# Kernel optimization log

Hardware: AMD Instinct MI355X
Metric: run time of the kernel (lower is better)

The kernel has to match this reference:

```python
import jax, jax.numpy as jnp
import numpy as np

SEQ, D_IN, D_OUT = 8192, 768, 64


def setup_inputs() -> dict:
    key = jax.random.key(0)
    k0, k1, k2, k3 = jax.random.split(key, 4)
    x = jax.random.normal(k0, (SEQ, D_IN), dtype=jnp.float32)
    # nn.Linear default init ~ U(-1/sqrt(d_in), 1/sqrt(d_in)); small scale keeps softmax stable
    s = 0.02
    Wq = jax.random.normal(k1, (D_IN, D_OUT), dtype=jnp.float32) * s
    Wk = jax.random.normal(k2, (D_IN, D_OUT), dtype=jnp.float32) * s
    Wv = jax.random.normal(k3, (D_IN, D_OUT), dtype=jnp.float32) * s
    return {"x": x, "Wq": Wq, "Wk": Wk, "Wv": Wv}


def reference(x, Wq, Wk, Wv):
    # queries/keys/values: [S, d_out]
    q = x @ Wq
    k = x @ Wk
    v = x @ Wv
    d_k = k.shape[-1]
    scores = q @ k.T / jnp.sqrt(jnp.asarray(d_k, x.dtype))  # [S, S]
    weights = jax.nn.softmax(scores, axis=-1)
    return weights @ v  # [S, d_out]
```

## Files before the change

### kernel.cpp

```cpp
#include <hip/hip_runtime.h>
#include <hip/hip_bf16.h>

#define SEQ  8192
#define DIN  768
#define DOUT 64

typedef __attribute__((ext_vector_type(8))) short short8;
typedef __attribute__((ext_vector_type(4))) short s16x4;
typedef __attribute__((ext_vector_type(4))) float f32x4;

__device__ inline unsigned short f2bf(float f) {
    __hip_bfloat16 h = __float2bfloat16(f);
    return __builtin_bit_cast(unsigned short, h);
}

__global__ __launch_bounds__(256) void wconv_kernel(
    const float* __restrict__ Wq, const float* __restrict__ Wk,
    const float* __restrict__ Wv, unsigned short* __restrict__ Wt) {
    int idx = blockIdx.x * 256 + threadIdx.x;
    int c = idx / DIN;
    int k = idx - c * DIN;
    int sel = c >> 6, cc = c & 63;
    const float* W = (sel == 0) ? Wq : ((sel == 1) ? Wk : Wv);
    float v = W[k * DOUT + cc];
    if (sel == 0) v *= 0.125f * 1.4426950408889634f;
    Wt[c * DIN + k] = f2bf(v);
}

__global__ __launch_bounds__(256) void proj_kernel(
    const float* __restrict__ x, const unsigned short* __restrict__ Wt,
    unsigned short* __restrict__ Q8, unsigned short* __restrict__ Kf,
    unsigned short* __restrict__ Vf) {
    __shared__ unsigned short xs[16 * 72];
    __shared__ unsigned short ws[192 * 72];

    const int tid  = threadIdx.x;
    const int m0   = blockIdx.x * 16;
    const int lane = tid & 63;
    const int w    = tid >> 6;
    const int g    = lane >> 4;
    const int l15  = lane & 15;

    f32x4 zero = {0.f, 0.f, 0.f, 0.f};
    f32x4 acc[3] = {zero, zero, zero};

    for (int kt = 0; kt < 12; ++kt) {
        const int k0 = kt * 64;
        {
            int r = tid >> 4, c4 = (tid & 15) * 4;
            float4 f = *reinterpret_cast<const float4*>(&x[(m0 + r) * DIN + k0 + c4]);
            s16x4 o4;
            o4[0] = (short)f2bf(f.x); o4[1] = (short)f2bf(f.y);
            o4[2] = (short)f2bf(f.z); o4[3] = (short)f2bf(f.w);
            *(s16x4*)&xs[r * 72 + c4] = o4;
        }
#pragma unroll
        for (int p = 0; p < 6; ++p) {
            int c    = p * 32 + (tid >> 3);
            int col8 = (tid & 7) * 8;
            *(short8*)&ws[c * 72 + col8] =
                *(const short8*)&Wt[c * DIN + k0 + col8];
        }
        __syncthreads();
        short8 a0 = *(short8*)&xs[l15 * 72 + g * 8];
        short8 a1 = *(short8*)&xs[l15 * 72 + g * 8 + 32];
#pragma unroll
        for (int i = 0; i < 3; ++i) {
            int nt = w * 3 + i;
            short8 b0 = *(short8*)&ws[(nt * 16 + l15) * 72 + g * 8];
            short8 b1 = *(short8*)&ws[(nt * 16 + l15) * 72 + g * 8 + 32];
            acc[i] = __builtin_amdgcn_mfma_f32_16x16x32_bf16(a0, b0, acc[i], 0, 0, 0);
            acc[i] = __builtin_amdgcn_mfma_f32_16x16x32_bf16(a1, b1, acc[i], 0, 0, 0);
        }
        __syncthreads();
    }
#pragma unroll
    for (int i = 0; i < 3; ++i) {
#pragma unroll
        for (int r = 0; r < 4; ++r) {
            int row = m0 + g * 4 + r;
            int col = (w * 3 + i) * 16 + l15;
            unsigned short b = f2bf(acc[i][r]);
            if (col < 64) {
                Q8[row * 64 + col] = b;
            } else if (col < 128) {
                int d  = col - 64;
                int t  = row >> 6, nt = (row >> 4) & 3, lk = row & 15;
                int h  = d >> 5, kg = (d >> 3) & 3, e = d & 7;
                Kf[(((t * 4 + nt) * 2 + h) * 64 + kg * 16 + lk) * 8 + e] = b;
            } else {
                int d  = col - 128;
                int kv = row;
                int t  = kv >> 6, k6 = kv & 63;
                int c  = k6 >> 5, r5 = k6 & 31;
                int hf = r5 >> 4, vg = (r5 >> 2) & 3, j = (r5 & 3) + hf * 4;
                int dn = d >> 4, lv = d & 15;
                Vf[(((t * 2 + c) * 4 + dn) * 64 + vg * 16 + lv) * 8 + j] = b;
            }
        }
    }
}

__global__ __launch_bounds__(256, 4) void flash_kernel(
    const unsigned short* __restrict__ Q8, const unsigned short* __restrict__ Kf,
    const unsigned short* __restrict__ Vf, float* __restrict__ Op,
    float* __restrict__ Mp, float* __restrict__ Lp, int ntiles) {
    const int tid  = threadIdx.x;
    const int w    = tid >> 6;
    const int lane = tid & 63;
    const int g    = lane >> 4;
    const int l15  = lane & 15;
    const int q0   = (blockIdx.x * 4 + w) * 32;
    const int nsub = ntiles * 2;
    const int sub0 = blockIdx.y * nsub;

    short8 qa[4];
#pragma unroll
    for (int qg = 0; qg < 2; ++qg) {
        qa[qg * 2 + 0] = *(const short8*)&Q8[(q0 + qg * 16 + l15) * 64 + g * 8];
        qa[qg * 2 + 1] = *(const short8*)&Q8[(q0 + qg * 16 + l15) * 64 + g * 8 + 32];
    }

    f32x4 zero = {0.f, 0.f, 0.f, 0.f};
    f32x4 o[2][4];
    float m[2]  = {-3e38f, -3e38f};
    float ln[2] = {0.f, 0.f};
#pragma unroll
    for (int qg = 0; qg < 2; ++qg)
#pragma unroll
        for (int dn = 0; dn < 4; ++dn) o[qg][dn] = zero;

    const unsigned short* kfp = Kf + (size_t)sub0 * 2048 + lane * 8;
    const unsigned short* vfp = Vf + (size_t)sub0 * 2048 + lane * 8;

    short8 kb[2][2];
#pragma unroll
    for (int nt = 0; nt < 2; ++nt)
#pragma unroll
        for (int h = 0; h < 2; ++h)
            kb[nt][h] = *(const short8*)&kfp[(nt * 2 + h) * 512];

    for (int i = 0; i < nsub; ++i) {
        f32x4 s[2][2];
#pragma unroll
        for (int qg = 0; qg < 2; ++qg)
#pragma unroll
            for (int nt = 0; nt < 2; ++nt) s[qg][nt] = zero;
#pragma unroll
        for (int nt = 0; nt < 2; ++nt) {
            s[0][nt] = __builtin_amdgcn_mfma_f32_16x16x32_bf16(kb[nt][0], qa[0], s[0][nt], 0, 0, 0);
            s[0][nt] = __builtin_amdgcn_mfma_f32_16x16x32_bf16(kb[nt][1], qa[1], s[0][nt], 0, 0, 0);
            s[1][nt] = __builtin_amdgcn_mfma_f32_16x16x32_bf16(kb[nt][0], qa[2], s[1][nt], 0, 0, 0);
            s[1][nt] = __builtin_amdgcn_mfma_f32_16x16x32_bf16(kb[nt][1], qa[3], s[1][nt], 0, 0, 0);
        }

        short8 vf[4];
#pragma unroll
        for (int dn = 0; dn < 4; ++dn)
            vf[dn] = *(const short8*)&vfp[(size_t)i * 2048 + dn * 512];

#pragma unroll
        for (int nt = 0; nt < 2; ++nt)
#pragma unroll
            for (int h = 0; h < 2; ++h)
                kb[nt][h] = *(const short8*)&kfp[(size_t)(i + 1) * 2048 + (nt * 2 + h) * 512];

        short8 pa[2];
#pragma unroll
        for (int qg = 0; qg < 2; ++qg) {
            float pm = fmaxf(
                fmaxf(fmaxf(s[qg][0][0], s[qg][0][1]), fmaxf(s[qg][0][2], s[qg][0][3])),
                fmaxf(fmaxf(s[qg][1][0], s[qg][1][1]), fmaxf(s[qg][1][2], s[qg][1][3])));
            if (__any(pm > m[qg] + 8.f)) {
                pm = fmaxf(pm, __shfl_xor(pm, 16));
                pm = fmaxf(pm, __shfl_xor(pm, 32));
                float mn = fmaxf(m[qg], pm);
                float a  = __builtin_amdgcn_exp2f(m[qg] - mn);
                m[qg] = mn;
                ln[qg] *= a;
#pragma unroll
                for (int dn = 0; dn < 4; ++dn) o[qg][dn] *= a;
            }
            float p[8];
#pragma unroll
            for (int nt = 0; nt < 2; ++nt)
#pragma unroll
                for (int r = 0; r < 4; ++r)
                    p[nt * 4 + r] = __builtin_amdgcn_exp2f(s[qg][nt][r] - m[qg]);
            ln[qg] += ((p[0] + p[1]) + (p[2] + p[3])) + ((p[4] + p[5]) + (p[6] + p[7]));
            short8 pk;
#pragma unroll
            for (int j = 0; j < 8; ++j) pk[j] = (short)f2bf(p[j]);
            pa[qg] = pk;
        }

#pragma unroll
        for (int dn = 0; dn < 4; ++dn) {
            o[0][dn] = __builtin_amdgcn_mfma_f32_16x16x32_bf16(vf[dn], pa[0], o[0][dn], 0, 0, 0);
            o[1][dn] = __builtin_amdgcn_mfma_f32_16x16x32_bf16(vf[dn], pa[1], o[1][dn], 0, 0, 0);
        }
    }

    const size_t sb = (size_t)blockIdx.y * SEQ;
#pragma unroll
    for (int qg = 0; qg < 2; ++qg) {
        float ps = ln[qg];
        ps += __shfl_xor(ps, 16);
        ps += __shfl_xor(ps, 32);
#pragma unroll
        for (int dn = 0; dn < 4; ++dn)
            *(f32x4*)&Op[(sb + q0 + qg * 16 + l15) * 64 + dn * 16 + 4 * g] = o[qg][dn];
        if (g == 0) {
            Mp[sb + q0 + qg * 16 + l15] = m[qg];
            Lp[sb + q0 + qg * 16 + l15] = ps;
        }
    }
}

__global__ __launch_bounds__(256) void reduce_kernel(
    const float* __restrict__ Op, const float* __restrict__ Mp,
    const float* __restrict__ Lp, float* __restrict__ Out, int NS) {
    int q = blockIdx.x * 4 + (threadIdx.x >> 6);
    int d = threadIdx.x & 63;
    float M = -3e38f;
    for (int s = 0; s < NS; ++s) M = fmaxf(M, Mp[s * SEQ + q]);
    float L = 0.f, acc = 0.f;
    for (int s = 0; s < NS; ++s) {
        float w = __builtin_amdgcn_exp2f(Mp[s * SEQ + q] - M);
        L   += Lp[s * SEQ + q] * w;
        acc += Op[((size_t)s * SEQ + q) * 64 + d] * w;
    }
    Out[q * 64 + d] = acc / L;
}

extern "C" void kernel_launch(void* const* d_in, const int* in_sizes, int n_in,
                              void* d_out, int out_size, void* d_ws, size_t ws_size,
                              hipStream_t stream) {
    const float* x  = (const float*)d_in[0];
    const float* Wq = (const float*)d_in[1];
    const float* Wk = (const float*)d_in[2];
    const float* Wv = (const float*)d_in[3];
    float* out = (float*)d_out;

    char* ws = (char*)d_ws;
    unsigned short* Wt = (unsigned short*)(ws);
    unsigned short* Q8 = (unsigned short*)(ws + 294912);
    unsigned short* Kf = (unsigned short*)(ws + 294912 + 1048576);
    unsigned short* Vf = (unsigned short*)(ws + 294912 + 2097152);
    const size_t fixed = 294912 + 3 * 1048576;

    int NS = 16;
    while (NS > 1 && fixed + (size_t)NS * (2097152 + 65536) > ws_size) NS >>= 1;
    float* Op = (float*)(ws + fixed);
    float* Mp = (float*)(ws + fixed + (size_t)NS * 2097152);
    float* Lp = (float*)(ws + fixed + (size_t)NS * 2097152 + (size_t)NS * 32768);
    const int ntiles = SEQ / (NS * 64);

    wconv_kernel<<<dim3(576), dim3(256), 0, stream>>>(Wq, Wk, Wv, Wt);
    proj_kernel<<<dim3(512), dim3(256), 0, stream>>>(x, Wt, Q8, Kf, Vf);
    flash_kernel<<<dim3(64, NS), dim3(256), 0, stream>>>(Q8, Kf, Vf, Op, Mp, Lp, ntiles);
    reduce_kernel<<<dim3(2048), dim3(256), 0, stream>>>(Op, Mp, Lp, out, NS);
}
```

Before: 61.54 us.

## Share K/V tiles via double-buffered LDS in flash kernel; enlarge projection row tile

In the flash kernel, each wave used to load the full K and V subtiles from global memory on its own. Now the four waves load one quarter each into double-buffered shared memory and synchronise every iteration, which cuts global/L2 traffic by four at the cost of a block barrier per subtile. The projection kernel now handles 32 rows per block instead of 16, with each wave covering 6 output column tiles. This halves the number of redundant weight-tile loads and the grid size. The per-iteration __syncthreads may reduce latency hiding, and the flash kernel now uses extra LDS, which could limit occupancy.

Measured after the change: 81.32 us. +32.1%, slower.

```diff
diff --git a/kernel.cpp b/kernel.cpp
--- a/kernel.cpp
+++ b/kernel.cpp
@@ -31,28 +31,31 @@
     const float* __restrict__ x, const unsigned short* __restrict__ Wt,
     unsigned short* __restrict__ Q8, unsigned short* __restrict__ Kf,
     unsigned short* __restrict__ Vf) {
-    __shared__ unsigned short xs[16 * 72];
+    __shared__ unsigned short xs[32 * 72];
     __shared__ unsigned short ws[192 * 72];
 
     const int tid  = threadIdx.x;
-    const int m0   = blockIdx.x * 16;
+    const int m0   = blockIdx.x * 32;
     const int lane = tid & 63;
     const int w    = tid >> 6;
+    const int rh   = w & 1;
+    const int ch   = w >> 1;
     const int g    = lane >> 4;
     const int l15  = lane & 15;
 
     f32x4 zero = {0.f, 0.f, 0.f, 0.f};
-    f32x4 acc[3] = {zero, zero, zero};
+    f32x4 acc[6] = {zero, zero, zero, zero, zero, zero};
 
     for (int kt = 0; kt < 12; ++kt) {
         const int k0 = kt * 64;
         {
-            int r = tid >> 4, c4 = (tid & 15) * 4;
-            float4 f = *reinterpret_cast<const float4*>(&x[(m0 + r) * DIN + k0 + c4]);
-            s16x4 o4;
-            o4[0] = (short)f2bf(f.x); o4[1] = (short)f2bf(f.y);
-            o4[2] = (short)f2bf(f.z); o4[3] = (short)f2bf(f.w);
-            *(s16x4*)&xs[r * 72 + c4] = o4;
+            int r = tid >> 3, c8 = (tid & 7) * 8;
+            const float4* src4 = reinterpret_cast<const float4*>(&x[(m0 + r) * DIN + k0 + c8]);
+            float4 f0 = src4[0], f1 = src4[1];
+            short8 o8;
+            o8[0]=(short)f2bf(f0.x); o8[1]=(short)f2bf(f0.y); o8[2]=(short)f2bf(f0.z); o8[3]=(short)f2bf(f0.w);
+            o8[4]=(short)f2bf(f1.x); o8[5]=(short)f2bf(f1.y); o8[6]=(short)f2bf(f1.z); o8[7]=(short)f2bf(f1.w);
+            *(short8*)&xs[r * 72 + c8] = o8;
         }
 #pragma unroll
         for (int p = 0; p < 6; ++p) {
@@ -62,11 +65,11 @@
                 *(const short8*)&Wt[c * DIN + k0 + col8];
         }
         __syncthreads();
-        short8 a0 = *(short8*)&xs[l15 * 72 + g * 8];
-        short8 a1 = *(short8*)&xs[l15 * 72 + g * 8 + 32];
-#pragma unroll
-        for (int i = 0; i < 3; ++i) {
-            int nt = w * 3 + i;
+        short8 a0 = *(short8*)&xs[(rh * 16 + l15) * 72 + g * 8];
+        short8 a1 = *(short8*)&xs[(rh * 16 + l15) * 72 + g * 8 + 32];
+#pragma unroll
+        for (int i = 0; i < 6; ++i) {
+            int nt = ch * 6 + i;
             short8 b0 = *(short8*)&ws[(nt * 16 + l15) * 72 + g * 8];
             short8 b1 = *(short8*)&ws[(nt * 16 + l15) * 72 + g * 8 + 32];
             acc[i] = __builtin_amdgcn_mfma_f32_16x16x32_bf16(a0, b0, acc[i], 0, 0, 0);
@@ -75,11 +78,11 @@
         __syncthreads();
     }
 #pragma unroll
-    for (int i = 0; i < 3; ++i) {
+    for (int i = 0; i < 6; ++i) {
 #pragma unroll
         for (int r = 0; r < 4; ++r) {
-            int row = m0 + g * 4 + r;
-            int col = (w * 3 + i) * 16 + l15;
+            int row = m0 + rh * 16 + g * 4 + r;
+            int col = (ch * 6 + i) * 16 + l15;
             unsigned short b = f2bf(acc[i][r]);
             if (col < 64) {
                 Q8[row * 64 + col] = b;
@@ -105,12 +108,15 @@
     const unsigned short* __restrict__ Q8, const unsigned short* __restrict__ Kf,
     const unsigned short* __restrict__ Vf, float* __restrict__ Op,
     float* __restrict__ Mp, float* __restrict__ Lp, int ntiles) {
+    __shared__ unsigned short lk[2][2048];
+    __shared__ unsigned short lv[2][2048];
+
     const int tid  = threadIdx.x;
     const int w    = tid >> 6;
     const int lane = tid & 63;
     const int g    = lane >> 4;
     const int l15  = lane & 15;
-    const int q0   = (blockIdx.x * 4 + w) * 32;
+    const int q0   = blockIdx.x * 128 + w * 32;
     const int nsub = ntiles * 2;
     const int sub0 = blockIdx.y * nsub;
 
@@ -130,17 +136,30 @@
 #pragma unroll
         for (int dn = 0; dn < 4; ++dn) o[qg][dn] = zero;
 
-    const unsigned short* kfp = Kf + (size_t)sub0 * 2048 + lane * 8;
-    const unsigned short* vfp = Vf + (size_t)sub0 * 2048 + lane * 8;
-
-    short8 kb[2][2];
-#pragma unroll
-    for (int nt = 0; nt < 2; ++nt)
-#pragma unroll
-        for (int h = 0; h < 2; ++h)
-            kb[nt][h] = *(const short8*)&kfp[(nt * 2 + h) * 512];
+    const unsigned short* ksrc = Kf + (size_t)sub0 * 2048 + w * 512 + lane * 8;
+    const unsigned short* vsrc = Vf + (size_t)sub0 * 2048 + w * 512 + lane * 8;
+    const int lslot = w * 512 + lane * 8;
+
+    short8 rk = *(const short8*)ksrc;
+    short8 rv = *(const short8*)vsrc;
+    *(short8*)&lk[0][lslot] = rk;
+    *(short8*)&lv[0][lslot] = rv;
+    __syncthreads();
 
     for (int i = 0; i < nsub; ++i) {
+        const int cur = i & 1;
+        if (i + 1 < nsub) {
+            rk = *(const short8*)&ksrc[(size_t)(i + 1) * 2048];
+            rv = *(const short8*)&vsrc[(size_t)(i + 1) * 2048];
+        }
+
+        short8 kb[2][2];
+#pragma unroll
+        for (int nt = 0; nt < 2; ++nt)
+#pragma unroll
+            for (int h = 0; h < 2; ++h)
+                kb[nt][h] = *(short8*)&lk[cur][(nt * 2 + h) * 512 + lane * 8];
+
         f32x4 s[2][2];
 #pragma unroll
         for (int qg = 0; qg < 2; ++qg)
@@ -154,16 +173,10 @@
             s[1][nt] = __builtin_amdgcn_mfma_f32_16x16x32_bf16(kb[nt][1], qa[3], s[1][nt], 0, 0, 0);
         }
 
-        short8 vf[4];
+        short8 vfr[4];
 #pragma unroll
         for (int dn = 0; dn < 4; ++dn)
-            vf[dn] = *(const short8*)&vfp[(size_t)i * 2048 + dn * 512];
-
-#pragma unroll
-        for (int nt = 0; nt < 2; ++nt)
-#pragma unroll
-            for (int h = 0; h < 2; ++h)
-                kb[nt][h] = *(const short8*)&kfp[(size_t)(i + 1) * 2048 + (nt * 2 + h) * 512];
+            vfr[dn] = *(short8*)&lv[cur][dn * 512 + lane * 8];
 
         short8 pa[2];
 #pragma unroll
@@ -196,9 +209,15 @@
 
 #pragma unroll
         for (int dn = 0; dn < 4; ++dn) {
-            o[0][dn] = __builtin_amdgcn_mfma_f32_16x16x32_bf16(vf[dn], pa[0], o[0][dn], 0, 0, 0);
-            o[1][dn] = __builtin_amdgcn_mfma_f32_16x16x32_bf16(vf[dn], pa[1], o[1][dn], 0, 0, 0);
-        }
+            o[0][dn] = __builtin_amdgcn_mfma_f32_16x16x32_bf16(vfr[dn], pa[0], o[0][dn], 0, 0, 0);
+            o[1][dn] = __builtin_amdgcn_mfma_f32_16x16x32_bf16(vfr[dn], pa[1], o[1][dn], 0, 0, 0);
+        }
+
+        if (i + 1 < nsub) {
+            *(short8*)&lk[cur ^ 1][lslot] = rk;
+            *(short8*)&lv[cur ^ 1][lslot] = rv;
+        }
+        __syncthreads();
     }
 
     const size_t sb = (size_t)blockIdx.y * SEQ;
@@ -257,7 +276,7 @@
     const int ntiles = SEQ / (NS * 64);
 
     wconv_kernel<<<dim3(576), dim3(256), 0, stream>>>(Wq, Wk, Wv, Wt);
-    proj_kernel<<<dim3(512), dim3(256), 0, stream>>>(x, Wt, Q8, Kf, Vf);
+    proj_kernel<<<dim3(256), dim3(256), 0, stream>>>(x, Wt, Q8, Kf, Vf);
     flash_kernel<<<dim3(64, NS), dim3(256), 0, stream>>>(Q8, Kf, Vf, Op, Mp, Lp, ntiles);
     reduce_kernel<<<dim3(2048), dim3(256), 0, stream>>>(Op, Mp, Lp, out, NS);
 }
```
